# Performance work log

Hardware: AMD Instinct MI355X
Metric: run time of the kernel (lower is better)

## Reference

```python
import jax, jax.numpy as jnp
import numpy as np

B, S, D, H, DFF = 2, 2048, 768, 12, 3072
DK = D // H
EPS = 1e-6
NEG = -1e9


def setup_inputs() -> dict:
    key = jax.random.key(0)
    ks = jax.random.split(key, 16)
    s = 1.0 / np.sqrt(D)
    inp = {
        'x': jax.random.normal(ks[0], (B, S, D), jnp.float32),
        'wq': jax.random.normal(ks[1], (D, D), jnp.float32) * s,
        'bq': jnp.zeros((D,), jnp.float32),
        'wk': jax.random.normal(ks[2], (D, D), jnp.float32) * s,
        'bk': jnp.zeros((D,), jnp.float32),
        'wv': jax.random.normal(ks[3], (D, D), jnp.float32) * s,
        'bv': jnp.zeros((D,), jnp.float32),
        'wo': jax.random.normal(ks[4], (D, D), jnp.float32) * s,
        'bo': jnp.zeros((D,), jnp.float32),
        'w1': jax.random.normal(ks[5], (D, DFF), jnp.float32) * s,
        'b1': jnp.zeros((DFF,), jnp.float32),
        'w2': jax.random.normal(ks[6], (DFF, D), jnp.float32) * (1.0 / np.sqrt(DFF)),
        'b2': jnp.zeros((D,), jnp.float32),
        'alpha1': jnp.ones((1,), jnp.float32),
        'beta1': jnp.zeros((1,), jnp.float32),
        'alpha2': jnp.ones((1,), jnp.float32),
        'beta2': jnp.zeros((1,), jnp.float32),
        'mask': jax.random.randint(ks[7], (1, 1, S, S), 0, 2, jnp.int32),
    }
    return inp


def layernorm(x, alpha, beta):
    # torch: mean and UNBIASED std (ddof=1), eps added to std (not variance)
    mean = jnp.mean(x, axis=-1, keepdims=True)
    std = jnp.std(x, axis=-1, keepdims=True, ddof=1)
    return alpha * (x - mean) / (std + EPS) + beta


def encoder_layer(x, wq, bq, wk, bk, wv, bv, wo, bo, w1, b1, w2, b2,
                  alpha1, beta1, alpha2, beta2, mask):
    # projections -> [B, H, S, DK]
    def split_heads(t):
        return t.reshape(B, S, H, DK).transpose(0, 2, 1, 3)
    q = split_heads(x @ wq + bq)
    k = split_heads(x @ wk + bk)
    v = split_heads(x @ wv + bv)
    scores = jnp.einsum('bhqd,bhkd->bhqk', q, k) / np.sqrt(DK)  # [B,H,S,S]
    scores = jnp.where(mask == 0, NEG, scores)
    attn = jax.nn.softmax(scores, axis=-1)
    ctx = jnp.einsum('bhqk,bhkd->bhqd', attn, v)
    ctx = ctx.transpose(0, 2, 1, 3).reshape(B, S, D)
    attn_out = ctx @ wo + bo
    x = layernorm(x + attn_out, alpha1, beta1)
    ff = jax.nn.relu(x @ w1 + b1) @ w2 + b2
    x = layernorm(x + ff, alpha2, beta2)
    return x


def reference(x, wq, bq, wk, bk, wv, bv, wo, bo, w1, b1, w2, b2,
              alpha1, beta1, alpha2, beta2, mask):
    return encoder_layer(x, wq, bq, wk, bk, wv, bv, wo, bo, w1, b1, w2, b2,
                         alpha1, beta1, alpha2, beta2, mask)
```

## Files before the change

kernel.cpp:

```cpp
#include <hip/hip_runtime.h>
#include <hip/hip_bf16.h>


typedef short short8 __attribute__((ext_vector_type(8)));
typedef float floatx4 __attribute__((ext_vector_type(4)));
typedef unsigned short ushort_t;
typedef ushort_t ushort4_t __attribute__((ext_vector_type(4)));

#define B_ 2
#define S_ 2048
#define D_ 768
#define H_ 12
#define DK_ 64
#define DFF_ 3072
#define M_ (B_ * S_)
#define RS_ (3 * D_)

#define LOG2E 1.44269504f
#define FMAX_SHIFT 16.0f

__device__ __forceinline__ float bf2f(ushort_t h) {
  union { unsigned int u; float f; } v; v.u = ((unsigned int)h) << 16; return v.f;
}
__device__ __forceinline__ ushort_t f2bf(float f) {
  union { float f; unsigned int u; } v; v.f = f;
  unsigned int u = v.u;
  unsigned int r = (u + 0x7fffu + ((u >> 16) & 1u)) >> 16;
  return (ushort_t)r;
}

__global__ __launch_bounds__(256) void transpose_f2b(
    const float* __restrict__ in, ushort_t* __restrict__ out, int K, int N) {
  __shared__ ushort_t t[32][33];
  const int nt = blockIdx.x * 32, kt = blockIdx.y * 32;
  const int tx = threadIdx.x, ty = threadIdx.y;
#pragma unroll
  for (int i = 0; i < 4; i++)
    t[ty + i * 8][tx] = f2bf(in[(size_t)(kt + ty + i * 8) * N + nt + tx]);
  __syncthreads();
#pragma unroll
  for (int i = 0; i < 4; i++)
    out[(size_t)(nt + ty + i * 8) * K + kt + tx] = t[tx][ty + i * 8];
}

__global__ __launch_bounds__(256) void transpose4_f2b(
    const float* __restrict__ wq, const float* __restrict__ wk,
    const float* __restrict__ wv, const float* __restrict__ wo,
    ushort_t* __restrict__ wTqkv, ushort_t* __restrict__ woT) {
  __shared__ ushort_t t[32][33];
  const int z = blockIdx.z;
  const float* in = (z == 0) ? wq : (z == 1) ? wk : (z == 2) ? wv : wo;
  ushort_t* out = (z < 3) ? (wTqkv + (size_t)z * D_ * D_) : woT;
  const int nt = blockIdx.x * 32, kt = blockIdx.y * 32;
  const int tx = threadIdx.x, ty = threadIdx.y;
#pragma unroll
  for (int i = 0; i < 4; i++)
    t[ty + i * 8][tx] = f2bf(in[(size_t)(kt + ty + i * 8) * D_ + nt + tx]);
  __syncthreads();
#pragma unroll
  for (int i = 0; i < 4; i++)
    out[(size_t)(nt + ty + i * 8) * D_ + kt + tx] = t[tx][ty + i * 8];
}

__global__ __launch_bounds__(256) void mask_to_biasp(
    const int* __restrict__ mask, ushort_t* __restrict__ out) {
  const int t = blockIdx.x * 256 + threadIdx.x;
  const int q = t >> 8;
  const int cc = t & 255;
  const int k0 = (cc >> 3) * 64;
  const int g = cc & 7, f = g >> 2, lq = g & 3;
  const int* mrow = mask + (size_t)q * S_ + k0;
  const ushort_t cm = f2bf(-1.4427e9f);
  const ushort_t cu = f2bf(-FMAX_SHIFT * LOG2E);
  short8 o;
#pragma unroll
  for (int n2 = 0; n2 < 2; n2++)
#pragma unroll
    for (int r = 0; r < 4; r++) {
      const int kpl = 32 * f + 16 * n2 + 4 * lq + r;
      o[n2 * 4 + r] = (short)((mrow[kpl] == 0) ? cm : cu);
    }
  *(short8*)(out + (size_t)q * S_ + k0 + g * 8) = o;
}

__global__ __launch_bounds__(256) void vtrans(
    const ushort_t* __restrict__ qkv, ushort_t* __restrict__ vt) {
  __shared__ __align__(16) ushort_t T[64 * 72];
  const int tid = threadIdx.x;
  const int bh = blockIdx.y, b = bh / H_, h = bh % H_;
  const int k0 = blockIdx.x * 64;
  const ushort_t* vbase = qkv + (size_t)(b * S_) * RS_ + 2 * D_ + h * DK_;
#pragma unroll
  for (int i = 0; i < 2; i++) {
    const int idx = tid + i * 256;
    const int r = idx >> 3, c = idx & 7;
    short8 vv = *(const short8*)(vbase + (size_t)(k0 + r) * RS_ + c * 8);
    const int sw = (r >> 3) ^ c;
#pragma unroll
    for (int j = 0; j < 8; j++)
      T[(c * 8 + j) * 72 + sw * 8 + (r & 7)] = (ushort_t)vv[j];
  }
  __syncthreads();
#pragma unroll
  for (int i = 0; i < 2; i++) {
    const int ch = tid + i * 256;
    const int d = ch >> 3, g = ch & 7, f = g >> 2, lq = g & 3;
    short8 o;
#pragma unroll
    for (int n2 = 0; n2 < 2; n2++)
#pragma unroll
      for (int r = 0; r < 4; r++) {
        const int kpl = 32 * f + 16 * n2 + 4 * lq + r;
        o[n2 * 4 + r] = (short)T[d * 72 + (((kpl >> 3) ^ (d >> 3)) * 8) + (kpl & 7)];
      }
    *(short8*)(vt + ((size_t)bh * 64 + d) * S_ + k0 + g * 8) = o;
  }
}

__global__ __launch_bounds__(256) void cvt_f2b(
    const float* __restrict__ in, ushort_t* __restrict__ out, int n) {
  const int i = (blockIdx.x * 256 + threadIdx.x) * 4;
  if (i >= n) return;
#pragma unroll
  for (int j = 0; j < 4; j++) out[i + j] = f2bf(in[i + j]);
}

__global__ void concat3(const float* __restrict__ a, const float* __restrict__ b,
                        const float* __restrict__ c, float* __restrict__ o, int n) {
  int i = blockIdx.x * 256 + threadIdx.x;
  if (i >= 3 * n) return;
  o[i] = (i < n) ? a[i] : (i < 2 * n ? b[i - n] : c[i - 2 * n]);
}

template <int BN, bool SPLIT>
__global__ __launch_bounds__(256) void gemm_bt_t(
    const ushort_t* __restrict__ A, const ushort_t* __restrict__ Bt,
    const float* __restrict__ bias, void* __restrict__ Cv,
    int M, int N, int K, int relu, int qcols, float qscale) {
  constexpr int WN = (BN == 128) ? 2 : 1;
  constexpr int WM = 4 / WN;
  constexpr int FI = 128 / WM / 16;
  constexpr int FJ = BN / WN / 16;
  constexpr int Z = SPLIT ? 2 : 1;
  __shared__ __align__(16) ushort_t Al[2][128 * 32];
  __shared__ __align__(16) ushort_t Bl[2][BN * 32];
  const int tid = threadIdx.x;
  const int w = tid >> 6, lane = tid & 63;
  const int wm = (WN == 2) ? (w >> 1) : w;
  const int wn = (WN == 2) ? (w & 1) : 0;
  const int lq = lane >> 4, lr = lane & 15;

  const int NT_n = N / BN;
  const int mg = M >> 10;
  const int lin = blockIdx.x;
  const int xcd = lin & 7, idx = lin >> 3;
  const int m_t = xcd * mg + idx / (NT_n * Z);
  const int rem = idx % (NT_n * Z);
  const int n_t = rem % NT_n;
  const int z   = rem / NT_n;
  const int m0 = m_t * 128, n0 = n_t * BN;

  int kBeg = 0, kEnd = K;
  if (SPLIT) { const int half = K >> 1; kBeg = z * half; kEnd = kBeg + half; }
  const int NT = (kEnd - kBeg) / 32;

  auto stage = [&](int kt, int s) {
    const int k0 = kBeg + kt * 32;
#pragma unroll
    for (int i = 0; i < 2; i++) {
      const int base = (w * 2 + i) * 512;
      const int e = base + lane * 8;
      const int row = e >> 5, col = e & 31;
      __builtin_amdgcn_global_load_lds(
          (const __attribute__((address_space(1))) void*)(A + (size_t)(m0 + row) * K + k0 + col),
          (__attribute__((address_space(3))) void*)(&Al[s][base]), 16, 0, 0);
    }
#pragma unroll
    for (int i = 0; i < BN / 64; i++) {
      const int base = (w * (BN / 64) + i) * 512;
      const int e = base + lane * 8;
      const int row = e >> 5, col = e & 31;
      __builtin_amdgcn_global_load_lds(
          (const __attribute__((address_space(1))) void*)(Bt + (size_t)(n0 + row) * K + k0 + col),
          (__attribute__((address_space(3))) void*)(&Bl[s][base]), 16, 0, 0);
    }
  };

  floatx4 acc[FI][FJ];
#pragma unroll
  for (int i = 0; i < FI; i++)
#pragma unroll
    for (int j = 0; j < FJ; j++) acc[i][j] = (floatx4){0.f, 0.f, 0.f, 0.f};

  stage(0, 0);
  for (int kt = 0; kt < NT; kt++) {
    const int s = kt & 1;
    __syncthreads();
    if (kt + 1 < NT) stage(kt + 1, s ^ 1);

    short8 af[FI], bf[FJ];
#pragma unroll
    for (int i = 0; i < FI; i++)
      af[i] = *(const short8*)&Al[s][(wm * (FI * 16) + i * 16 + lr) * 32 + lq * 8];
#pragma unroll
    for (int j = 0; j < FJ; j++)
      bf[j] = *(const short8*)&Bl[s][(wn * (FJ * 16) + j * 16 + lr) * 32 + lq * 8];
#pragma unroll
    for (int i = 0; i < FI; i++)
#pragma unroll
      for (int j = 0; j < FJ; j++)
        acc[i][j] = __builtin_amdgcn_mfma_f32_16x16x32_bf16(af[i], bf[j], acc[i][j], 0, 0, 0);
  }

#pragma unroll
  for (int i = 0; i < FI; i++) {
    const int m = m0 + wm * (FI * 16) + i * 16 + lq * 4;
#pragma unroll
    for (int j = 0; j < FJ; j++) {
      const int n = n0 + wn * (FJ * 16) + j * 16 + lr;
      if (SPLIT) {
        ushort_t* P = (ushort_t*)Cv + (size_t)z * M * N;
#pragma unroll
        for (int r = 0; r < 4; r++)
          P[(size_t)(m + r) * N + n] = f2bf(acc[i][j][r]);
      } else {
        const float bv = bias[n];
#pragma unroll
        for (int r = 0; r < 4; r++) {
          float v = acc[i][j][r] + bv;
          if (n < qcols) v *= qscale;
          if (relu) v = v > 0.f ? v : 0.f;
          ((ushort_t*)Cv)[(size_t)(m + r) * N + n] = f2bf(v);
        }
      }
    }
  }
}

__global__ __launch_bounds__(256, 3) void flash_attn(
    const ushort_t* __restrict__ qkv, const ushort_t* __restrict__ vt,
    const ushort_t* __restrict__ maskp, ushort_t* __restrict__ ctx) {
  __shared__ __align__(16) ushort_t lds[2][3][64 * 64];
  const int tid = threadIdx.x;
  const int w = tid >> 6, lane = tid & 63;
  const int lq = lane >> 4, lr = lane & 15;
  const int blk = blockIdx.x;
  const int bh = blk % (B_ * H_), qb = blk / (B_ * H_);
  const int b = bh / H_, h = bh % H_;
  const int q0 = qb * 64;
  const ushort_t* qbase = qkv + (size_t)(b * S_) * RS_ + h * DK_;
  const ushort_t* kbase = qbase + D_;
  const ushort_t* vtb   = vt + (size_t)bh * DK_ * S_;
  const ushort_t* mb    = maskp + (size_t)q0 * S_;

  short8 qfr[2];
#pragma unroll
  for (int f = 0; f < 2; f++)
    qfr[f] = *(const short8*)(
        qbase + (size_t)(q0 + w * 16 + lr) * RS_ + f * 32 + lq * 8);

  auto stage = [&](int k0, int s) {
#pragma unroll
    for (int i = 0; i < 2; i++) {
      const int id = i * 256 + tid;
      const int row = id >> 3;
      const int cc = ((id & 7) ^ (row & 7)) * 8;
      const int dbase = (i * 256 + w * 64) * 8;
      __builtin_amdgcn_global_load_lds(
          (const __attribute__((address_space(1))) void*)(kbase + (size_t)(k0 + row) * RS_ + cc),
          (__attribute__((address_space(3))) void*)(&lds[s][0][dbase]), 16, 0, 0);
      __builtin_amdgcn_global_load_lds(
          (const __attribute__((address_space(1))) void*)(vtb + (size_t)row * S_ + k0 + cc),
          (__attribute__((address_space(3))) void*)(&lds[s][1][dbase]), 16, 0, 0);
      __builtin_amdgcn_global_load_lds(
          (const __attribute__((address_space(1))) void*)(mb + (size_t)row * S_ + k0 + cc),
          (__attribute__((address_space(3))) void*)(&lds[s][2][dbase]), 16, 0, 0);
    }
  };

  floatx4 oacc[4];
#pragma unroll
  for (int dt = 0; dt < 4; dt++) oacc[dt] = (floatx4){0.f, 0.f, 0.f, 0.f};
  float li = 0.f;

  stage(0, 0);
  __syncthreads();

  const int sw8 = lr & 7;
  const int c0 = (lq ^ sw8) * 8;
  const int c1 = ((4 + lq) ^ sw8) * 8;

  for (int t = 0; t < S_ / 64; t++) {
    const int s = t & 1;
    stage((t + 1) * 64, s ^ 1);

    const ushort_t* kl = &lds[s][0][0];
    const ushort_t* vl = &lds[s][1][0];
    const ushort_t* ml = &lds[s][2][0];

    const int mrow = (w * 16 + lr) * 64;
    short8 bb0 = *(const short8*)(ml + mrow + c0);
    short8 bb1 = *(const short8*)(ml + mrow + c1);

    floatx4 sacc[4];
#pragma unroll
    for (int n = 0; n < 4; n++) sacc[n] = (floatx4){0.f, 0.f, 0.f, 0.f};
#pragma unroll
    for (int n = 0; n < 4; n++) {
      const int krow = (n * 16 + lr) * 64;
      short8 a0 = *(const short8*)(kl + krow + c0);
      short8 a1 = *(const short8*)(kl + krow + c1);
      sacc[n] = __builtin_amdgcn_mfma_f32_16x16x32_bf16(a0, qfr[0], sacc[n], 0, 0, 0);
      sacc[n] = __builtin_amdgcn_mfma_f32_16x16x32_bf16(a1, qfr[1], sacc[n], 0, 0, 0);
    }

    short8 pf[2];
#pragma unroll
    for (int f = 0; f < 2; f++) {
      const short8 bb = f ? bb1 : bb0;
      union { __hip_bfloat162 h2[4]; short8 v; } u;
#pragma unroll
      for (int jj = 0; jj < 4; jj++) {
        const int e0 = jj * 2, e1 = jj * 2 + 1;
        float2 p2;
        p2.x = __builtin_amdgcn_exp2f(sacc[2 * f + (e0 >> 2)][e0 & 3] + bf2f((ushort_t)bb[e0]));
        p2.y = __builtin_amdgcn_exp2f(sacc[2 * f + (e1 >> 2)][e1 & 3] + bf2f((ushort_t)bb[e1]));
        li += p2.x + p2.y;
        u.h2[jj] = __float22bfloat162_rn(p2);
      }
      pf[f] = u.v;
    }

#pragma unroll
    for (int dt = 0; dt < 4; dt++) {
      const int vrow = (dt * 16 + lr) * 64;
      short8 v0 = *(const short8*)(vl + vrow + c0);
      short8 v1 = *(const short8*)(vl + vrow + c1);
      oacc[dt] = __builtin_amdgcn_mfma_f32_16x16x32_bf16(v0, pf[0], oacc[dt], 0, 0, 0);
      oacc[dt] = __builtin_amdgcn_mfma_f32_16x16x32_bf16(v1, pf[1], oacc[dt], 0, 0, 0);
    }
    __syncthreads();
  }

  li += __shfl_xor(li, 16);
  li += __shfl_xor(li, 32);
  const float inv = 1.f / (li + 1e-37f);

  const size_t row = (size_t)(b * S_ + q0 + w * 16 + lr) * D_ + h * DK_;
#pragma unroll
  for (int dt = 0; dt < 4; dt++) {
    ushort4_t o;
#pragma unroll
    for (int r = 0; r < 4; r++) o[r] = f2bf(oacc[dt][r] * inv);
    *(ushort4_t*)(ctx + row + dt * 16 + lq * 4) = o;
  }
}

template <bool XF, bool OF>
__global__ __launch_bounds__(256) void add_ln_comb(
    const void* __restrict__ xv, const ushort_t* __restrict__ P0,
    const ushort_t* __restrict__ P1, const float* __restrict__ cb,
    const float* __restrict__ alpha, const float* __restrict__ beta,
    void* __restrict__ outv) {
  const int row = blockIdx.x, tid = threadIdx.x;
  const int w = tid >> 6, lane = tid & 63;
  __shared__ float red[8];
  float v[3];
#pragma unroll
  for (int i = 0; i < 3; i++) {
    const int c = tid + i * 256;
    const size_t idx = (size_t)row * D_ + c;
    float xv_;
    if (XF) xv_ = ((const float*)xv)[idx];
    else    xv_ = bf2f(((const ushort_t*)xv)[idx]);
    v[i] = xv_ + (bf2f(P0[idx]) + bf2f(P1[idx]) + cb[c]);
  }
  float s = v[0] + v[1] + v[2];
#pragma unroll
  for (int off = 1; off < 64; off <<= 1) s += __shfl_xor(s, off);
  if (lane == 0) red[w] = s;
  __syncthreads();
  const float mean = (red[0] + red[1] + red[2] + red[3]) / (float)D_;
  float d = 0.f;
#pragma unroll
  for (int i = 0; i < 3; i++) { const float t = v[i] - mean; d += t * t; }
#pragma unroll
  for (int off = 1; off < 64; off <<= 1) d += __shfl_xor(d, off);
  if (lane == 0) red[4 + w] = d;
  __syncthreads();
  const float var = (red[4] + red[5] + red[6] + red[7]) / (float)(D_ - 1);
  const float inv = 1.f / (sqrtf(var) + 1e-6f);
  const float a = alpha[0] * inv, bt = beta[0];
#pragma unroll
  for (int i = 0; i < 3; i++) {
    const int c = tid + i * 256;
    const float o = a * (v[i] - mean) + bt;
    if (OF) ((float*)outv)[(size_t)row * D_ + c] = o;
    else    ((ushort_t*)outv)[(size_t)row * D_ + c] = f2bf(o);
  }
}

extern "C" void kernel_launch(void* const* d_in, const int* in_sizes, int n_in,
                              void* d_out, int out_size, void* d_ws, size_t ws_size,
                              hipStream_t stream) {
  const float* x   = (const float*)d_in[0];
  const float* wq  = (const float*)d_in[1];
  const float* bq  = (const float*)d_in[2];
  const float* wk  = (const float*)d_in[3];
  const float* bk  = (const float*)d_in[4];
  const float* wv  = (const float*)d_in[5];
  const float* bv  = (const float*)d_in[6];
  const float* wo  = (const float*)d_in[7];
  const float* bo  = (const float*)d_in[8];
  const float* w1  = (const float*)d_in[9];
  const float* b1  = (const float*)d_in[10];
  const float* w2  = (const float*)d_in[11];
  const float* b2  = (const float*)d_in[12];
  const float* a1  = (const float*)d_in[13];
  const float* be1 = (const float*)d_in[14];
  const float* a2  = (const float*)d_in[15];
  const float* be2 = (const float*)d_in[16];
  const int*   msk = (const int*)d_in[17];

  const size_t E_xb    = 0;
  const size_t E_wTqkv = E_xb    + (size_t)M_ * D_;
  const size_t E_woT   = E_wTqkv + (size_t)3 * D_ * D_;
  const size_t E_w1T   = E_woT   + (size_t)D_ * D_;
  const size_t E_w2T   = E_w1T   + (size_t)DFF_ * D_;
  const size_t E_bqkv  = E_w2T   + (size_t)D_ * DFF_;
  const size_t E_qkv   = E_bqkv  + (size_t)2 * 3 * D_;
  const size_t E_ctx   = E_qkv   + (size_t)M_ * 3 * D_;
  const size_t E_attn  = E_ctx   + (size_t)M_ * D_;
  const size_t E_x1    = E_attn  + (size_t)M_ * D_;
  const size_t E_h1    = E_x1    + (size_t)M_ * D_;
  const size_t E_ff    = E_h1    + (size_t)M_ * DFF_;
  const size_t E_total = E_ff    + (size_t)M_ * D_;
  if (ws_size < E_total * sizeof(ushort_t)) return;

  ushort_t* ws    = (ushort_t*)d_ws;
  ushort_t* xb    = ws + E_xb;
  ushort_t* wTqkv = ws + E_wTqkv;
  ushort_t* woT   = ws + E_woT;
  ushort_t* w1T   = ws + E_w1T;
  ushort_t* w2T   = ws + E_w2T;
  float*    bqkv  = (float*)(ws + E_bqkv);
  ushort_t* qkv   = ws + E_qkv;
  ushort_t* ctx   = ws + E_ctx;
  ushort_t* x1    = ws + E_x1;
  ushort_t* h1    = ws + E_h1;
  ushort_t* maskp = ws + E_h1;
  ushort_t* vt    = ws + E_h1 + (size_t)S_ * S_;
  ushort_t* Pattn = ws + E_h1;
  ushort_t* Pff2  = ws + E_qkv;

  const float SCALE_Q = 0.125f * LOG2E;

  const dim3 tb(32, 8);
  transpose4_f2b<<<dim3(24, 24, 4), tb, 0, stream>>>(wq, wk, wv, wo, wTqkv, woT);
  transpose_f2b<<<dim3(96, 24), tb, 0, stream>>>(w1, w1T, D_, DFF_);
  transpose_f2b<<<dim3(24, 96), tb, 0, stream>>>(w2, w2T, DFF_, D_);
  mask_to_biasp<<<(S_ * S_ / 8) / 256, 256, 0, stream>>>(msk, maskp);
  concat3<<<9, 256, 0, stream>>>(bq, bk, bv, bqkv, D_);
  cvt_f2b<<<(M_ * D_ / 4 + 255) / 256, 256, 0, stream>>>(x, xb, M_ * D_);

  gemm_bt_t<64, false><<<1152, 256, 0, stream>>>(
      xb, wTqkv, bqkv, qkv, M_, 3 * D_, D_, 0, D_, SCALE_Q);
  vtrans<<<dim3(S_ / 64, B_ * H_), 256, 0, stream>>>(qkv, vt);
  flash_attn<<<(B_ * H_) * (S_ / 64), 256, 0, stream>>>(qkv, vt, maskp, ctx);
  gemm_bt_t<64, true><<<768, 256, 0, stream>>>(
      ctx, woT, nullptr, Pattn, M_, D_, D_, 0, 0, 1.f);
  add_ln_comb<true, false><<<M_, 256, 0, stream>>>(
      x, Pattn, Pattn + (size_t)M_ * D_, bo, a1, be1, x1);
  gemm_bt_t<128, false><<<768, 256, 0, stream>>>(
      x1, w1T, b1, h1, M_, DFF_, D_, 1, 0, 1.f);
  gemm_bt_t<64, true><<<768, 256, 0, stream>>>(
      h1, w2T, nullptr, Pff2, M_, D_, DFF_, 0, 0, 1.f);
  add_ln_comb<false, true><<<M_, 256, 0, stream>>>(
      x1, Pff2, Pff2 + (size_t)M_ * D_, b2, a2, be2, d_out);
}
```

Measured before the change: 303.5 us.

## Split flash-attention waves over query and key halves with MFMA row sums

Each wave now handles 32 query rows and half of each 64-key tile, so every K and V fragment loaded from LDS feeds two MFMAs and LDS fragment traffic drops. The mask bias is preloaded into the score accumulator, and the softmax denominator is computed with an MFMA against a ones vector rather than with scalar adds and shuffles. The two key-half partial outputs are combined through LDS at the end, which costs an extra barrier, an LDS exchange, and more accumulator registers per wave. The prefetch past the last tile is also skipped.

New measurement: 304.6 us. No clear change (+0.4%).

```diff
diff --git a/kernel.cpp b/kernel.cpp
--- a/kernel.cpp
+++ b/kernel.cpp
@@ -243,6 +243,7 @@
   __shared__ __align__(16) ushort_t lds[2][3][64 * 64];
   const int tid = threadIdx.x;
   const int w = tid >> 6, lane = tid & 63;
+  const int wq = w >> 1, wk = w & 1;
   const int lq = lane >> 4, lr = lane & 15;
   const int blk = blockIdx.x;
   const int bh = blk % (B_ * H_), qb = blk / (B_ * H_);
@@ -253,11 +254,13 @@
   const ushort_t* vtb   = vt + (size_t)bh * DK_ * S_;
   const ushort_t* mb    = maskp + (size_t)q0 * S_;
 
-  short8 qfr[2];
-#pragma unroll
-  for (int f = 0; f < 2; f++)
-    qfr[f] = *(const short8*)(
-        qbase + (size_t)(q0 + w * 16 + lr) * RS_ + f * 32 + lq * 8);
+  short8 qfr[2][2];
+#pragma unroll
+  for (int qf = 0; qf < 2; qf++)
+#pragma unroll
+    for (int f = 0; f < 2; f++)
+      qfr[qf][f] = *(const short8*)(
+          qbase + (size_t)(q0 + wq * 32 + qf * 16 + lr) * RS_ + f * 32 + lq * 8);
 
   auto stage = [&](int k0, int s) {
 #pragma unroll
@@ -278,10 +281,16 @@
     }
   };
 
-  floatx4 oacc[4];
-#pragma unroll
-  for (int dt = 0; dt < 4; dt++) oacc[dt] = (floatx4){0.f, 0.f, 0.f, 0.f};
-  float li = 0.f;
+  floatx4 oacc[2][4], oli[2];
+#pragma unroll
+  for (int qf = 0; qf < 2; qf++) {
+    oli[qf] = (floatx4){0.f, 0.f, 0.f, 0.f};
+#pragma unroll
+    for (int dt = 0; dt < 4; dt++) oacc[qf][dt] = (floatx4){0.f, 0.f, 0.f, 0.f};
+  }
+  short8 ones;
+#pragma unroll
+  for (int j = 0; j < 8; j++) ones[j] = (short)0x3F80;
 
   stage(0, 0);
   __syncthreads();
@@ -289,70 +298,106 @@
   const int sw8 = lr & 7;
   const int c0 = (lq ^ sw8) * 8;
   const int c1 = ((4 + lq) ^ sw8) * 8;
-
-  for (int t = 0; t < S_ / 64; t++) {
+  const int cW = ((4 * wk + lq) ^ sw8) * 8;
+
+  constexpr int NT = S_ / 64;
+  for (int t = 0; t < NT; t++) {
     const int s = t & 1;
-    stage((t + 1) * 64, s ^ 1);
+    if (t + 1 < NT) stage((t + 1) * 64, s ^ 1);
 
     const ushort_t* kl = &lds[s][0][0];
     const ushort_t* vl = &lds[s][1][0];
     const ushort_t* ml = &lds[s][2][0];
 
-    const int mrow = (w * 16 + lr) * 64;
-    short8 bb0 = *(const short8*)(ml + mrow + c0);
-    short8 bb1 = *(const short8*)(ml + mrow + c1);
-
-    floatx4 sacc[4];
-#pragma unroll
-    for (int n = 0; n < 4; n++) sacc[n] = (floatx4){0.f, 0.f, 0.f, 0.f};
-#pragma unroll
-    for (int n = 0; n < 4; n++) {
-      const int krow = (n * 16 + lr) * 64;
+    floatx4 sacc[2][2];
+#pragma unroll
+    for (int qf = 0; qf < 2; qf++) {
+      const short8 bb = *(const short8*)(ml + (wq * 32 + qf * 16 + lr) * 64 + cW);
+#pragma unroll
+      for (int n2 = 0; n2 < 2; n2++)
+#pragma unroll
+        for (int r = 0; r < 4; r++)
+          sacc[qf][n2][r] = bf2f((ushort_t)bb[n2 * 4 + r]);
+    }
+
+#pragma unroll
+    for (int n2 = 0; n2 < 2; n2++) {
+      const int krow = ((2 * wk + n2) * 16 + lr) * 64;
       short8 a0 = *(const short8*)(kl + krow + c0);
       short8 a1 = *(const short8*)(kl + krow + c1);
-      sacc[n] = __builtin_amdgcn_mfma_f32_16x16x32_bf16(a0, qfr[0], sacc[n], 0, 0, 0);
-      sacc[n] = __builtin_amdgcn_mfma_f32_16x16x32_bf16(a1, qfr[1], sacc[n], 0, 0, 0);
+#pragma unroll
+      for (int qf = 0; qf < 2; qf++) {
+        sacc[qf][n2] = __builtin_amdgcn_mfma_f32_16x16x32_bf16(a0, qfr[qf][0], sacc[qf][n2], 0, 0, 0);
+        sacc[qf][n2] = __builtin_amdgcn_mfma_f32_16x16x32_bf16(a1, qfr[qf][1], sacc[qf][n2], 0, 0, 0);
+      }
     }
 
     short8 pf[2];
 #pragma unroll
-    for (int f = 0; f < 2; f++) {
-      const short8 bb = f ? bb1 : bb0;
+    for (int qf = 0; qf < 2; qf++) {
       union { __hip_bfloat162 h2[4]; short8 v; } u;
 #pragma unroll
       for (int jj = 0; jj < 4; jj++) {
         const int e0 = jj * 2, e1 = jj * 2 + 1;
         float2 p2;
-        p2.x = __builtin_amdgcn_exp2f(sacc[2 * f + (e0 >> 2)][e0 & 3] + bf2f((ushort_t)bb[e0]));
-        p2.y = __builtin_amdgcn_exp2f(sacc[2 * f + (e1 >> 2)][e1 & 3] + bf2f((ushort_t)bb[e1]));
-        li += p2.x + p2.y;
+        p2.x = __builtin_amdgcn_exp2f(sacc[qf][e0 >> 2][e0 & 3]);
+        p2.y = __builtin_amdgcn_exp2f(sacc[qf][e1 >> 2][e1 & 3]);
         u.h2[jj] = __float22bfloat162_rn(p2);
       }
-      pf[f] = u.v;
+      pf[qf] = u.v;
     }
 
 #pragma unroll
     for (int dt = 0; dt < 4; dt++) {
-      const int vrow = (dt * 16 + lr) * 64;
-      short8 v0 = *(const short8*)(vl + vrow + c0);
-      short8 v1 = *(const short8*)(vl + vrow + c1);
-      oacc[dt] = __builtin_amdgcn_mfma_f32_16x16x32_bf16(v0, pf[0], oacc[dt], 0, 0, 0);
-      oacc[dt] = __builtin_amdgcn_mfma_f32_16x16x32_bf16(v1, pf[1], oacc[dt], 0, 0, 0);
-    }
+      const short8 vfr = *(const short8*)(vl + (dt * 16 + lr) * 64 + cW);
+#pragma unroll
+      for (int qf = 0; qf < 2; qf++)
+        oacc[qf][dt] = __builtin_amdgcn_mfma_f32_16x16x32_bf16(vfr, pf[qf], oacc[qf][dt], 0, 0, 0);
+    }
+#pragma unroll
+    for (int qf = 0; qf < 2; qf++)
+      oli[qf] = __builtin_amdgcn_mfma_f32_16x16x32_bf16(ones, pf[qf], oli[qf], 0, 0, 0);
+
     __syncthreads();
   }
 
-  li += __shfl_xor(li, 16);
-  li += __shfl_xor(li, 32);
-  const float inv = 1.f / (li + 1e-37f);
-
-  const size_t row = (size_t)(b * S_ + q0 + w * 16 + lr) * D_ + h * DK_;
-#pragma unroll
-  for (int dt = 0; dt < 4; dt++) {
-    ushort4_t o;
-#pragma unroll
-    for (int r = 0; r < 4; r++) o[r] = f2bf(oacc[dt][r] * inv);
-    *(ushort4_t*)(ctx + row + dt * 16 + lq * 4) = o;
+  float* ex = (float*)&lds[0][0][0];
+  if (wk == 1) {
+    float* dst = ex + (size_t)(wq * 64 + lane) * 37;
+#pragma unroll
+    for (int qf = 0; qf < 2; qf++)
+#pragma unroll
+      for (int dt = 0; dt < 4; dt++)
+#pragma unroll
+        for (int r = 0; r < 4; r++)
+          dst[qf * 16 + dt * 4 + r] = oacc[qf][dt][r];
+    dst[32] = oli[0][0];
+    dst[33] = oli[1][0];
+  }
+  __syncthreads();
+  if (wk == 0) {
+    const float* src = ex + (size_t)(wq * 64 + lane) * 37;
+#pragma unroll
+    for (int qf = 0; qf < 2; qf++)
+#pragma unroll
+      for (int dt = 0; dt < 4; dt++)
+#pragma unroll
+        for (int r = 0; r < 4; r++)
+          oacc[qf][dt][r] += src[qf * 16 + dt * 4 + r];
+    const float inv0 = 1.f / (oli[0][0] + src[32] + 1e-30f);
+    const float inv1 = 1.f / (oli[1][0] + src[33] + 1e-30f);
+#pragma unroll
+    for (int qf = 0; qf < 2; qf++) {
+      const float inv = qf ? inv1 : inv0;
+      const size_t row = (size_t)(b * S_ + q0 + wq * 32 + qf * 16 + lr) * D_ + h * DK_;
+#pragma unroll
+      for (int dt = 0; dt < 4; dt++) {
+        ushort4_t o;
+#pragma unroll
+        for (int r = 0; r < 4; r++) o[r] = f2bf(oacc[qf][dt][r] * inv);
+        *(ushort4_t*)(ctx + row + dt * 16 + lq * 4) = o;
+      }
+    }
   }
 }
 
```
